# Kernel tuning notes

Measured on AMD Instinct MI355X. Metric: run time of the kernel, lower is better.

The kernel has to match this reference:

```python
import jax, jax.numpy as jnp
import numpy as np

EPS = 1e-5  # torch BatchNorm default

def _conv(x, w, pad):
    return jax.lax.conv_general_dilated(x, w, window_strides=(1, 1), padding=pad,
                                        dimension_numbers=('NCHW', 'OIHW', 'NCHW'))

def _bn(x, g, b, m, v):
    # eval-mode BatchNorm2d over channel axis 1 of NCHW
    scale = g / jnp.sqrt(v + EPS)
    return x * scale[None, :, None, None] + (b - m * scale)[None, :, None, None]

def _bn1d(x, g, b, m, v):
    scale = g / jnp.sqrt(v + EPS)
    return x * scale[None, :] + (b - m * scale)[None, :]

def _prelu(x, a):
    # torch PReLU with num_parameters=1 (scalar slope, init 0.25)
    return jnp.where(x >= 0, x, a * x)

def setup_inputs():
    key = jax.random.key(0)
    ks = jax.random.split(key, 10)
    B, H, W = 256, 600, 19
    C1, C2 = 40, 40
    x = jax.random.normal(ks[0], (B, H, W), jnp.float32)
    w1 = jax.random.normal(ks[1], (C1, 1, 29, 1), jnp.float32) * 0.1
    w2 = jax.random.normal(ks[2], (C2, C1, 1, 19), jnp.float32) * 0.1
    fc1_w = jax.random.uniform(ks[3], (80, 1560), jnp.float32, -0.005, 0.005)
    fc2_w = jax.random.uniform(ks[4], (2, 80), jnp.float32, -0.005, 0.005)
    def bn_params(k, n):
        k1, k2 = jax.random.split(k)
        return (jnp.ones((n,), jnp.float32), jnp.zeros((n,), jnp.float32),
                jax.random.normal(k1, (n,), jnp.float32) * 0.1,
                jax.random.uniform(k2, (n,), jnp.float32, 0.5, 1.5))
    bn1_g, bn1_b, bn1_m, bn1_v = bn_params(ks[5], C1)
    bn2_g, bn2_b, bn2_m, bn2_v = bn_params(ks[6], C2)
    bn3_g, bn3_b, bn3_m, bn3_v = bn_params(ks[7], 80)
    a1 = jnp.full((1,), 0.25, jnp.float32)
    a2 = jnp.full((1,), 0.25, jnp.float32)
    a3 = jnp.full((1,), 0.25, jnp.float32)
    return dict(x=x, w1=w1, bn1_g=bn1_g, bn1_b=bn1_b, bn1_m=bn1_m, bn1_v=bn1_v, a1=a1,
                w2=w2, bn2_g=bn2_g, bn2_b=bn2_b, bn2_m=bn2_m, bn2_v=bn2_v, a2=a2,
                fc1_w=fc1_w, bn3_g=bn3_g, bn3_b=bn3_b, bn3_m=bn3_m, bn3_v=bn3_v, a3=a3,
                fc2_w=fc2_w)

def reference(x, w1, bn1_g, bn1_b, bn1_m, bn1_v, a1,
              w2, bn2_g, bn2_b, bn2_m, bn2_v, a2,
              fc1_w, bn3_g, bn3_b, bn3_m, bn3_v, a3, fc2_w):
    h = x[:, None, :, :]                                  # [B,1,600,19]
    # conv1: inputs NOT binarized, weights sign-binarized
    h = _conv(h, jnp.sign(w1), [(14, 14), (0, 0)])         # [B,40,600,19]
    h = _prelu(_bn(h, bn1_g, bn1_b, bn1_m, bn1_v), a1)
    # conv2: inputs and weights binarized
    h = _conv(jnp.sign(h), jnp.sign(w2), [(0, 0), (0, 0)])  # [B,40,600,1]
    h = _prelu(_bn(h, bn2_g, bn2_b, bn2_m, bn2_v), a2)
    # AvgPool2d kernel (30,1) stride (15,1)
    h = jax.lax.reduce_window(h, 0.0, jax.lax.add, (1, 1, 30, 1), (1, 1, 15, 1), 'VALID') / 30.0  # [B,40,39,1]
    h = h.reshape(h.shape[0], -1)                          # [B,1560]
    # fc1: binarized input/weight; BatchNorm1d; PReLU; dropout is identity in eval
    h = jnp.sign(h) @ jnp.sign(fc1_w).T                    # [B,80]
    h = _prelu(_bn1d(h, bn3_g, bn3_b, bn3_m, bn3_v), a3)
    out = jnp.sign(h) @ jnp.sign(fc2_w).T                  # [B,2]
    return out
```

## Files before the change

### kernel.cpp

```cpp
#include <hip/hip_runtime.h>
#include <stdint.h>

#define B_ 256
#define H_ 600
#define W_ 19
#define C1_ 40
#define C2_ 40
#define KH_ 29
#define PAD_ 14
#define NW_ 760
#define NWORDS_ 12
#define NJ_ 39
#define FIN_ 1560
#define FOUT_ 80
#define FCW_ 25
#define XST2 328
#define HS_ 300

__device__ __forceinline__ float fsgn(float x){ return (x > 0.f) ? 1.f : ((x < 0.f) ? -1.f : 0.f); }
__device__ __forceinline__ int8_t isgn(float x){ return (int8_t)((x > 0.f) - (x < 0.f)); }

__global__ void k0_setup(const float* __restrict__ w1, const float* __restrict__ w2,
                         const float* __restrict__ fc1w, const float* __restrict__ fc2w,
                         const float* __restrict__ g1, const float* __restrict__ b1,
                         const float* __restrict__ m1, const float* __restrict__ v1,
                         const float* __restrict__ g2, const float* __restrict__ b2,
                         const float* __restrict__ m2, const float* __restrict__ v2,
                         const float* __restrict__ g3, const float* __restrict__ b3,
                         const float* __restrict__ m3, const float* __restrict__ v3,
                         float* __restrict__ w1s, uint64_t* __restrict__ w2m,
                         uint64_t* __restrict__ fc1p, int8_t* __restrict__ fc2s,
                         float* __restrict__ bnp)
{
  int tid = blockIdx.x * blockDim.x + threadIdx.x;
  int np  = gridDim.x * blockDim.x;
  int lane = threadIdx.x & 63;
  int gw   = tid >> 6;
  int nw   = np >> 6;

  for (int i = tid; i < C1_*KH_; i += np) w1s[i] = fsgn(w1[i]);

  for (int v = gw; v < C2_*24; v += nw){
    int c2 = v / 24, r = v % 24;
    int neg = r / 12, wd = r % 12;
    int idx = wd*64 + lane;
    float val = 0.f;
    if (idx < NW_){
      int c1 = idx % 40, w = idx / 40;
      val = w2[c2*NW_ + c1*W_ + w];
    }
    unsigned long long m = __ballot(neg ? (val < 0.f) : (val > 0.f));
    if (lane == 0) w2m[c2*24 + r] = m;
  }
  for (int v = gw; v < FOUT_*2*FCW_; v += nw){
    int o = v / (2*FCW_), r = v % (2*FCW_);
    int neg = r / FCW_, wd = r % FCW_;
    int e = wd*64 + lane;
    float val = (e < FIN_) ? fc1w[o*FIN_ + e] : 0.f;
    unsigned long long m = __ballot(neg ? (val < 0.f) : (val > 0.f));
    if (lane == 0) fc1p[o*(2*FCW_) + r] = m;
  }
  for (int i = tid; i < 2*FOUT_; i += np) fc2s[i] = isgn(fc2w[i]);
  for (int i = tid; i < C1_; i += np){
    float s = __fdiv_rn(g1[i], __fsqrt_rn(__fadd_rn(v1[i], 1e-5f)));
    bnp[i] = s; bnp[40+i] = __fsub_rn(b1[i], __fmul_rn(m1[i], s));
  }
  for (int i = tid; i < C2_; i += np){
    float s = __fdiv_rn(g2[i], __fsqrt_rn(__fadd_rn(v2[i], 1e-5f)));
    bnp[80+i] = s; bnp[120+i] = __fsub_rn(b2[i], __fmul_rn(m2[i], s));
  }
  for (int i = tid; i < FOUT_; i += np){
    float s = __fdiv_rn(g3[i], __fsqrt_rn(__fadd_rn(v3[i], 1e-5f)));
    bnp[160+i] = s; bnp[240+i] = __fsub_rn(b3[i], __fmul_rn(m3[i], s));
  }
}

__global__ __launch_bounds__(768, 6) void k1_conv1(const float* __restrict__ x,
                                                   const float* __restrict__ w1s,
                                                   const float* __restrict__ bnp,
                                                   uint64_t* __restrict__ s1bits)
{
  __shared__ float xs[W_ * XST2];
  __shared__ float wl[KH_ * 40];
  int b = blockIdx.x, t = blockIdx.y;
  int h0 = HS_ * t;
  const float* xb = x + (size_t)b * H_ * W_;
  for (int i = threadIdx.x; i < XST2 * W_; i += 768){
    int r = i / W_, w = i % W_;
    int gh = h0 - PAD_ + r;
    xs[w*XST2 + r] = (gh >= 0 && gh < H_) ? xb[gh*W_ + w] : 0.f;
  }
  for (int i = threadIdx.x; i < KH_*40; i += 768){
    int k = i / 40, c1 = i % 40;
    wl[i] = w1s[c1*KH_ + k];
  }
  __syncthreads();

  int tid  = threadIdx.x;
  int lane = tid & 63, wave = tid >> 6;
  bool valid = (tid < NW_);
  int c1 = tid % 40;
  int w  = valid ? (tid / 40) : 18;

  float scale = bnp[c1], bias = bnp[40 + c1];
  const float* xcol = &xs[w * XST2];
  const float* wcol = &wl[c1];
  uint64_t* bbase = s1bits + ((size_t)b * H_ + h0) * 24;

  for (int c = 0; c < 25; ++c){
    float xr[40];
    const float4* xp = (const float4*)&xcol[12*c];
    #pragma unroll
    for (int q = 0; q < 10; ++q){
      float4 v = xp[q];
      xr[4*q+0] = v.x; xr[4*q+1] = v.y; xr[4*q+2] = v.z; xr[4*q+3] = v.w;
    }
    float acc[12];
    #pragma unroll
    for (int dh = 0; dh < 12; ++dh) acc[dh] = 0.f;
    #pragma unroll
    for (int k = 0; k < KH_; ++k){
      float wk = wcol[k*40];
      #pragma unroll
      for (int dh = 0; dh < 12; ++dh)
        acc[dh] = __builtin_fmaf(wk, xr[dh + k], acc[dh]);
    }
    #pragma unroll
    for (int dh = 0; dh < 12; ++dh){
      float z = __fadd_rn(__fmul_rn(acc[dh], scale), bias);
      unsigned long long pos = __ballot(valid && (z > 0.f));
      unsigned long long neg = __ballot(valid && (z < 0.f));
      if (lane == 0){
        uint64_t* d = bbase + (size_t)(12*c + dh) * 24;
        d[wave] = pos; d[wave + 12] = neg;
      }
    }
  }
}

__global__ __launch_bounds__(256) void k2_conv2pool(const uint64_t* __restrict__ s1bits,
                                                    const uint64_t* __restrict__ w2m_g,
                                                    const float* __restrict__ bnp,
                                                    const float* __restrict__ a2p,
                                                    int8_t* __restrict__ sp)
{
  __shared__ uint64_t s1P[90][12];
  __shared__ uint64_t s1M[90][12];
  __shared__ uint64_t w2p[12][C2_];
  __shared__ float    z2[C2_][91];
  __shared__ int      nzr[90];
  int t = blockIdx.x, b = blockIdx.y;
  int h0 = 75 * t;
  int rows = (H_ - h0 < 90) ? (H_ - h0) : 90;

  const uint64_t* src = s1bits + ((size_t)b * H_ + h0) * 24;
  for (int i = threadIdx.x; i < rows*12; i += 256){
    int r = i / 12, wd = i % 12;
    uint64_t P = src[r*24 + wd], N = src[r*24 + 12 + wd];
    s1P[r][wd] = P; s1M[r][wd] = P | N;
  }
  for (int i = threadIdx.x; i < 12*C2_; i += 256){
    int c2 = i / 12, wd = i % 12;
    w2p[wd][c2] = w2m_g[c2*24 + wd];
  }
  __syncthreads();
  if (threadIdx.x < rows){
    int r = threadIdx.x, nz = 0;
    #pragma unroll
    for (int wd = 0; wd < NWORDS_; ++wd) nz += __popcll(s1M[r][wd]);
    nzr[r] = nz;
  }
  __syncthreads();

  float alpha = a2p[0];
  for (int o = threadIdx.x; o < rows*C2_; o += 256){
    int hl = o / C2_, c2 = o % C2_;
    int d = 0;
    #pragma unroll
    for (int wd = 0; wd < NWORDS_; ++wd)
      d += __popcll(s1M[hl][wd] & (s1P[hl][wd] ^ w2p[wd][c2]));
    int y = nzr[hl] - 2*d;
    float u = __fadd_rn(__fmul_rn((float)y, bnp[c2]), bnp[40 + c2]);
    z2[c2][hl] = (u >= 0.f) ? u : __fmul_rn(alpha, u);
  }
  __syncthreads();

  int nj = NJ_ - 5*t; if (nj > 5) nj = 5;
  for (int o = threadIdx.x; o < nj*C2_; o += 256){
    int jj = o / C2_, c2 = o % C2_;
    float s = 0.f;
    int base = 15 * jj;
    #pragma unroll
    for (int r = 0; r < 30; ++r) s = __fadd_rn(s, z2[c2][base + r]);
    sp[(size_t)b * FIN_ + c2 * NJ_ + 5*t + jj] = (int8_t)((s > 0.f) - (s < 0.f));
  }
}

__global__ __launch_bounds__(128) void k3_fc(const int8_t* __restrict__ sp,
                                             const uint64_t* __restrict__ fc1p,
                                             const int8_t* __restrict__ fc2s,
                                             const float* __restrict__ bnp,
                                             const float* __restrict__ a3p,
                                             float* __restrict__ out)
{
  __shared__ uint64_t spP[FCW_], spN[FCW_];
  __shared__ int z3[FOUT_];
  int b = blockIdx.x;
  int lane = threadIdx.x & 63, wave = threadIdx.x >> 6;
  const int8_t* spb = sp + (size_t)b * FIN_;
  for (int wd = wave; wd < FCW_; wd += 2){
    int e = wd*64 + lane;
    int v = (e < FIN_) ? (int)spb[e] : 0;
    unsigned long long p = __ballot(v > 0);
    unsigned long long n = __ballot(v < 0);
    if (lane == 0){ spP[wd] = p; spN[wd] = n; }
  }
  __syncthreads();
  float alpha = a3p[0];
  if (threadIdx.x < FOUT_){
    int o = threadIdx.x;
    const uint64_t* wp = fc1p + o * (2*FCW_);
    int acc = 0;
    #pragma unroll
    for (int wd = 0; wd < FCW_; ++wd){
      uint64_t P = spP[wd], N = spN[wd];
      uint64_t WP = wp[wd], WN = wp[FCW_ + wd];
      acc += __popcll(P & WP) + __popcll(N & WN) - __popcll(P & WN) - __popcll(N & WP);
    }
    float u = __fadd_rn(__fmul_rn((float)acc, bnp[o]), bnp[80 + o]);
    float z = (u >= 0.f) ? u : __fmul_rn(alpha, u);
    z3[o] = (z > 0.f) - (z < 0.f);
  }
  __syncthreads();
  if (threadIdx.x < 2){
    int k = threadIdx.x;
    int acc = 0;
    for (int o = 0; o < FOUT_; ++o) acc += z3[o] * (int)fc2s[k * FOUT_ + o];
    out[b*2 + k] = (float)acc;
  }
}

extern "C" void kernel_launch(void* const* d_in, const int* in_sizes, int n_in,
                              void* d_out, int out_size, void* d_ws, size_t ws_size,
                              hipStream_t stream)
{
  const float* x    = (const float*)d_in[0];
  const float* w1   = (const float*)d_in[1];
  const float* g1   = (const float*)d_in[2];
  const float* b1   = (const float*)d_in[3];
  const float* m1   = (const float*)d_in[4];
  const float* v1   = (const float*)d_in[5];
  const float* a1   = (const float*)d_in[6];   (void)a1;
  const float* w2   = (const float*)d_in[7];
  const float* g2   = (const float*)d_in[8];
  const float* b2   = (const float*)d_in[9];
  const float* m2   = (const float*)d_in[10];
  const float* v2   = (const float*)d_in[11];
  const float* a2   = (const float*)d_in[12];
  const float* fc1w = (const float*)d_in[13];
  const float* g3   = (const float*)d_in[14];
  const float* b3   = (const float*)d_in[15];
  const float* m3   = (const float*)d_in[16];
  const float* v3   = (const float*)d_in[17];
  const float* a3   = (const float*)d_in[18];
  const float* fc2w = (const float*)d_in[19];

  char* ws = (char*)d_ws;
  uint64_t* s1bits = (uint64_t*)(ws);
  uint64_t* w2m    = (uint64_t*)(ws + 29491200);
  float*    w1s    = (float*)   (ws + 29498880);
  float*    bnp    = (float*)   (ws + 29503520);
  int8_t*   sp     = (int8_t*)  (ws + 29504800);
  uint64_t* fc1p   = (uint64_t*)(ws + 29904160);
  int8_t*   fc2s   = (int8_t*)  (ws + 29936160);

  k0_setup<<<dim3(128), dim3(256), 0, stream>>>(w1, w2, fc1w, fc2w,
                                                g1, b1, m1, v1,
                                                g2, b2, m2, v2,
                                                g3, b3, m3, v3,
                                                w1s, w2m, fc1p, fc2s, bnp);
  k1_conv1<<<dim3(B_, 2), dim3(768), 0, stream>>>(x, w1s, bnp, s1bits);
  k2_conv2pool<<<dim3(8, B_), dim3(256), 0, stream>>>(s1bits, w2m, bnp + 80, a2, sp);
  k3_fc<<<dim3(B_), dim3(128), 0, stream>>>(sp, fc1p, fc2s, bnp + 160, a3, (float*)d_out);
}
```

Baseline: 257.5 us.

## Use packed FMA in conv1, interleave sign bitplanes, fuse conv2 with pooling per window

Conv1 now keeps the binarized weights in registers as duplicated pairs and uses packed two-wide FMA on even/odd row pairs, dropping the shared weight table. It writes interleaved (pos, nonzero) bit words with 128-bit stores. Conv2 no longer needs a separate P|N pass or a shared z2 buffer: each thread loads its channel's weight mask into registers and accumulates a pooling window directly, using 8 windows per block over 5 blocks. This adds register pressure, lowers the occupancy hint, and makes overlapping window rows be recomputed.

```diff
diff --git a/kernel.cpp b/kernel.cpp
--- a/kernel.cpp
+++ b/kernel.cpp
@@ -17,6 +17,8 @@
 #define XST2 328
 #define HS_ 300
 
+typedef float v2f __attribute__((ext_vector_type(2)));
+
 __device__ __forceinline__ float fsgn(float x){ return (x > 0.f) ? 1.f : ((x < 0.f) ? -1.f : 0.f); }
 __device__ __forceinline__ int8_t isgn(float x){ return (int8_t)((x > 0.f) - (x < 0.f)); }
 
@@ -40,17 +42,16 @@
 
   for (int i = tid; i < C1_*KH_; i += np) w1s[i] = fsgn(w1[i]);
 
-  for (int v = gw; v < C2_*24; v += nw){
-    int c2 = v / 24, r = v % 24;
-    int neg = r / 12, wd = r % 12;
+  for (int v = gw; v < C2_*NWORDS_; v += nw){
+    int c2 = v / NWORDS_, wd = v % NWORDS_;
     int idx = wd*64 + lane;
     float val = 0.f;
     if (idx < NW_){
       int c1 = idx % 40, w = idx / 40;
       val = w2[c2*NW_ + c1*W_ + w];
     }
-    unsigned long long m = __ballot(neg ? (val < 0.f) : (val > 0.f));
-    if (lane == 0) w2m[c2*24 + r] = m;
+    unsigned long long m = __ballot(val > 0.f);
+    if (lane == 0) w2m[c2*NWORDS_ + wd] = m;
   }
   for (int v = gw; v < FOUT_*2*FCW_; v += nw){
     int o = v / (2*FCW_), r = v % (2*FCW_);
@@ -75,13 +76,22 @@
   }
 }
 
-__global__ __launch_bounds__(768, 6) void k1_conv1(const float* __restrict__ x,
+#define FMA2(a,b,c) __builtin_elementwise_fma(a,b,c)
+#define KE(k) { v2f wk = wt2[k]; \
+  a0 = FMA2(wk, E[(k)/2+0], a0); a1 = FMA2(wk, E[(k)/2+1], a1); \
+  a2 = FMA2(wk, E[(k)/2+2], a2); a3 = FMA2(wk, E[(k)/2+3], a3); \
+  a4 = FMA2(wk, E[(k)/2+4], a4); a5 = FMA2(wk, E[(k)/2+5], a5); }
+#define KO(k) { v2f wk = wt2[k]; \
+  a0 = FMA2(wk, O[((k)-1)/2+0], a0); a1 = FMA2(wk, O[((k)-1)/2+1], a1); \
+  a2 = FMA2(wk, O[((k)-1)/2+2], a2); a3 = FMA2(wk, O[((k)-1)/2+3], a3); \
+  a4 = FMA2(wk, O[((k)-1)/2+4], a4); a5 = FMA2(wk, O[((k)-1)/2+5], a5); }
+
+__global__ __launch_bounds__(768, 3) void k1_conv1(const float* __restrict__ x,
                                                    const float* __restrict__ w1s,
                                                    const float* __restrict__ bnp,
                                                    uint64_t* __restrict__ s1bits)
 {
   __shared__ float xs[W_ * XST2];
-  __shared__ float wl[KH_ * 40];
   int b = blockIdx.x, t = blockIdx.y;
   int h0 = HS_ * t;
   const float* xb = x + (size_t)b * H_ * W_;
@@ -90,10 +100,6 @@
     int gh = h0 - PAD_ + r;
     xs[w*XST2 + r] = (gh >= 0 && gh < H_) ? xb[gh*W_ + w] : 0.f;
   }
-  for (int i = threadIdx.x; i < KH_*40; i += 768){
-    int k = i / 40, c1 = i % 40;
-    wl[i] = w1s[c1*KH_ + k];
-  }
   __syncthreads();
 
   int tid  = threadIdx.x;
@@ -102,97 +108,102 @@
   int c1 = tid % 40;
   int w  = valid ? (tid / 40) : 18;
 
+  v2f wt2[KH_];
+  #pragma unroll
+  for (int k = 0; k < KH_; ++k){ float wv = w1s[c1*KH_ + k]; wt2[k] = (v2f){wv, wv}; }
   float scale = bnp[c1], bias = bnp[40 + c1];
+  if (!valid){ scale = __builtin_nanf(""); bias = scale; }
   const float* xcol = &xs[w * XST2];
-  const float* wcol = &wl[c1];
   uint64_t* bbase = s1bits + ((size_t)b * H_ + h0) * 24;
 
   for (int c = 0; c < 25; ++c){
-    float xr[40];
+    v2f E[20];
     const float4* xp = (const float4*)&xcol[12*c];
     #pragma unroll
     for (int q = 0; q < 10; ++q){
       float4 v = xp[q];
-      xr[4*q+0] = v.x; xr[4*q+1] = v.y; xr[4*q+2] = v.z; xr[4*q+3] = v.w;
-    }
-    float acc[12];
-    #pragma unroll
-    for (int dh = 0; dh < 12; ++dh) acc[dh] = 0.f;
-    #pragma unroll
-    for (int k = 0; k < KH_; ++k){
-      float wk = wcol[k*40];
-      #pragma unroll
-      for (int dh = 0; dh < 12; ++dh)
-        acc[dh] = __builtin_fmaf(wk, xr[dh + k], acc[dh]);
-    }
-    #pragma unroll
-    for (int dh = 0; dh < 12; ++dh){
-      float z = __fadd_rn(__fmul_rn(acc[dh], scale), bias);
-      unsigned long long pos = __ballot(valid && (z > 0.f));
-      unsigned long long neg = __ballot(valid && (z < 0.f));
+      E[2*q]   = (v2f){v.x, v.y};
+      E[2*q+1] = (v2f){v.z, v.w};
+    }
+    v2f O[19];
+    #pragma unroll
+    for (int m = 0; m < 19; ++m) O[m] = (v2f){E[m].y, E[m+1].x};
+
+    v2f a0 = (v2f)0.f, a1 = (v2f)0.f, a2 = (v2f)0.f,
+        a3 = (v2f)0.f, a4 = (v2f)0.f, a5 = (v2f)0.f;
+    KE(0)  KO(1)  KE(2)  KO(3)  KE(4)  KO(5)  KE(6)  KO(7)  KE(8)  KO(9)
+    KE(10) KO(11) KE(12) KO(13) KE(14) KO(15) KE(16) KO(17) KE(18) KO(19)
+    KE(20) KO(21) KE(22) KO(23) KE(24) KO(25) KE(26) KO(27) KE(28)
+
+    v2f accs[6] = {a0, a1, a2, a3, a4, a5};
+    #pragma unroll
+    for (int j = 0; j < 6; ++j){
+      float zx = __fadd_rn(__fmul_rn(accs[j].x, scale), bias);
+      float zy = __fadd_rn(__fmul_rn(accs[j].y, scale), bias);
+      unsigned long long px = __ballot(zx > 0.f);
+      unsigned long long nx = __ballot(zx < 0.f);
+      unsigned long long py = __ballot(zy > 0.f);
+      unsigned long long ny = __ballot(zy < 0.f);
       if (lane == 0){
-        uint64_t* d = bbase + (size_t)(12*c + dh) * 24;
-        d[wave] = pos; d[wave + 12] = neg;
+        int h = 12*c + 2*j;
+        ulonglong2 v0; v0.x = px; v0.y = px | nx;
+        ulonglong2 v1; v1.x = py; v1.y = py | ny;
+        *(ulonglong2*)(bbase + (size_t)h     * 24 + wave*2) = v0;
+        *(ulonglong2*)(bbase + (size_t)(h+1) * 24 + wave*2) = v1;
       }
     }
   }
 }
 
-__global__ __launch_bounds__(256) void k2_conv2pool(const uint64_t* __restrict__ s1bits,
+__global__ __launch_bounds__(320) void k2_conv2pool(const uint64_t* __restrict__ s1bits,
                                                     const uint64_t* __restrict__ w2m_g,
                                                     const float* __restrict__ bnp,
                                                     const float* __restrict__ a2p,
                                                     int8_t* __restrict__ sp)
 {
-  __shared__ uint64_t s1P[90][12];
-  __shared__ uint64_t s1M[90][12];
-  __shared__ uint64_t w2p[12][C2_];
-  __shared__ float    z2[C2_][91];
-  __shared__ int      nzr[90];
+  __shared__ uint64_t st[135][NWORDS_][2];
+  __shared__ int nz[136];
   int t = blockIdx.x, b = blockIdx.y;
-  int h0 = 75 * t;
-  int rows = (H_ - h0 < 90) ? (H_ - h0) : 90;
-
-  const uint64_t* src = s1bits + ((size_t)b * H_ + h0) * 24;
-  for (int i = threadIdx.x; i < rows*12; i += 256){
-    int r = i / 12, wd = i % 12;
-    uint64_t P = src[r*24 + wd], N = src[r*24 + 12 + wd];
-    s1P[r][wd] = P; s1M[r][wd] = P | N;
-  }
-  for (int i = threadIdx.x; i < 12*C2_; i += 256){
-    int c2 = i / 12, wd = i % 12;
-    w2p[wd][c2] = w2m_g[c2*24 + wd];
-  }
-  __syncthreads();
-  if (threadIdx.x < rows){
-    int r = threadIdx.x, nz = 0;
-    #pragma unroll
-    for (int wd = 0; wd < NWORDS_; ++wd) nz += __popcll(s1M[r][wd]);
-    nzr[r] = nz;
-  }
-  __syncthreads();
-
-  float alpha = a2p[0];
-  for (int o = threadIdx.x; o < rows*C2_; o += 256){
-    int hl = o / C2_, c2 = o % C2_;
-    int d = 0;
-    #pragma unroll
-    for (int wd = 0; wd < NWORDS_; ++wd)
-      d += __popcll(s1M[hl][wd] & (s1P[hl][wd] ^ w2p[wd][c2]));
-    int y = nzr[hl] - 2*d;
-    float u = __fadd_rn(__fmul_rn((float)y, bnp[c2]), bnp[40 + c2]);
-    z2[c2][hl] = (u >= 0.f) ? u : __fmul_rn(alpha, u);
-  }
-  __syncthreads();
-
-  int nj = NJ_ - 5*t; if (nj > 5) nj = 5;
-  for (int o = threadIdx.x; o < nj*C2_; o += 256){
-    int jj = o / C2_, c2 = o % C2_;
-    float s = 0.f;
-    int base = 15 * jj;
-    #pragma unroll
-    for (int r = 0; r < 30; ++r) s = __fadd_rn(s, z2[c2][base + r]);
-    sp[(size_t)b * FIN_ + c2 * NJ_ + 5*t + jj] = (int8_t)((s > 0.f) - (s < 0.f));
+  int j0 = 8*t;
+  int nwin = NJ_ - j0; if (nwin > 8) nwin = 8;
+  int r0 = 15*j0;
+  int rows = H_ - r0; if (rows > 135) rows = 135;
+  int tid = threadIdx.x;
+
+  const ulonglong2* src = (const ulonglong2*)(s1bits + ((size_t)b * H_ + r0) * 24);
+  ulonglong2* dst = (ulonglong2*)st;
+  for (int i = tid; i < rows*NWORDS_; i += 320) dst[i] = src[i];
+  __syncthreads();
+  for (int r = tid; r < rows; r += 320){
+    int s = 0;
+    #pragma unroll
+    for (int wd = 0; wd < NWORDS_; ++wd) s += __popcll(st[r][wd][1]);
+    nz[r] = s;
+  }
+  __syncthreads();
+
+  int c2 = tid % 40, jl = tid / 40;
+  if (jl < nwin){
+    uint64_t WP[NWORDS_];
+    #pragma unroll
+    for (int wd = 0; wd < NWORDS_; ++wd) WP[wd] = w2m_g[c2*NWORDS_ + wd];
+    float s2 = bnp[c2], t2 = bnp[40 + c2], alpha = a2p[0];
+    float psum = 0.f;
+    int rbase = 15*jl;
+    for (int rr = 0; rr < 30; ++rr){
+      int r = rbase + rr;
+      int d = 0;
+      #pragma unroll
+      for (int wd = 0; wd < NWORDS_; ++wd){
+        ulonglong2 pm = *(const ulonglong2*)&st[r][wd][0];
+        d += __popcll(pm.y & (pm.x ^ WP[wd]));
+      }
+      int y = nz[r] - 2*d;
+      float u = __fadd_rn(__fmul_rn((float)y, s2), t2);
+      float z = (u >= 0.f) ? u : __fmul_rn(alpha, u);
+      psum = __fadd_rn(psum, z);
+    }
+    sp[(size_t)b * FIN_ + c2 * NJ_ + (j0 + jl)] = (int8_t)((psum > 0.f) - (psum < 0.f));
   }
 }
 
@@ -268,11 +279,11 @@
   char* ws = (char*)d_ws;
   uint64_t* s1bits = (uint64_t*)(ws);
   uint64_t* w2m    = (uint64_t*)(ws + 29491200);
-  float*    w1s    = (float*)   (ws + 29498880);
-  float*    bnp    = (float*)   (ws + 29503520);
-  int8_t*   sp     = (int8_t*)  (ws + 29504800);
-  uint64_t* fc1p   = (uint64_t*)(ws + 29904160);
-  int8_t*   fc2s   = (int8_t*)  (ws + 29936160);
+  float*    w1s    = (float*)   (ws + 29495040);
+  float*    bnp    = (float*)   (ws + 29499680);
+  int8_t*   sp     = (int8_t*)  (ws + 29500960);
+  uint64_t* fc1p   = (uint64_t*)(ws + 29900320);
+  int8_t*   fc2s   = (int8_t*)  (ws + 29932320);
 
   k0_setup<<<dim3(128), dim3(256), 0, stream>>>(w1, w2, fc1w, fc2w,
                                                 g1, b1, m1, v1,
@@ -280,6 +291,6 @@
                                                 g3, b3, m3, v3,
                                                 w1s, w2m, fc1p, fc2s, bnp);
   k1_conv1<<<dim3(B_, 2), dim3(768), 0, stream>>>(x, w1s, bnp, s1bits);
-  k2_conv2pool<<<dim3(8, B_), dim3(256), 0, stream>>>(s1bits, w2m, bnp + 80, a2, sp);
+  k2_conv2pool<<<dim3(5, B_), dim3(320), 0, stream>>>(s1bits, w2m, bnp + 80, a2, sp);
   k3_fc<<<dim3(B_), dim3(128), 0, stream>>>(sp, fc1p, fc2s, bnp + 160, a3, (float*)d_out);
 }
```

After: 244.5 us. 5.1% less time.
